# Performance work log

Measured on AMD Instinct MI355X. Metric: run time of the kernel, lower is better.

Reference implementation:

```python
import jax, jax.numpy as jnp
import numpy as np

N, E, G = 200000, 800000, 8192
IN, H, D, EXTRA = 128, 4, 64, 16


def setup_inputs() -> dict:
    key = jax.random.key(0)
    ks = jax.random.split(key, 24)
    inp = {
        'feats_node': jax.random.normal(ks[0], (N, IN), jnp.float32),
        'feats_graph': jax.random.normal(ks[1], (G, EXTRA), jnp.float32),
        'src': jax.random.randint(ks[2], (E,), 0, N, jnp.int32),
        'dst': jax.random.randint(ks[3], (E,), 0, N, jnp.int32),
        'graph_ids': jnp.sort(jax.random.randint(ks[4], (N,), 0, G, jnp.int32)),
        # GAT layer 1: fc [H*D, IN], attn [H, D], bias zeros (DGL default)
        'fc1_w': 0.5 * jax.random.normal(ks[5], (H * D, IN), jnp.float32),
        'attn_l1': 0.5 * jax.random.normal(ks[6], (H, D), jnp.float32),
        'attn_r1': 0.5 * jax.random.normal(ks[7], (H, D), jnp.float32),
        'bias1': jnp.zeros((H * D,), jnp.float32),
        # GAT layer 2
        'fc2_w': 0.5 * jax.random.normal(ks[8], (H * D, H * D), jnp.float32),
        'attn_l2': 0.5 * jax.random.normal(ks[9], (H, D), jnp.float32),
        'attn_r2': 0.5 * jax.random.normal(ks[10], (H, D), jnp.float32),
        'bias2': jnp.zeros((H * D,), jnp.float32),
        # GAT layer 3: 1 head
        'fc3_w': 0.5 * jax.random.normal(ks[11], (D, H * D), jnp.float32),
        'attn_l3': 0.5 * jax.random.normal(ks[12], (1, D), jnp.float32),
        'attn_r3': 0.5 * jax.random.normal(ks[13], (1, D), jnp.float32),
        'bias3': jnp.zeros((D,), jnp.float32),
        # readout score
        'score_w': 0.5 * jax.random.normal(ks[14], (1, D), jnp.float32),
        'score_b': jnp.zeros((1,), jnp.float32),
        # MLP: [D+EXTRA -> 2D -> D -> 1]
        'mlp_w1': 0.5 * jax.random.normal(ks[15], (2 * D, D + EXTRA), jnp.float32),
        'mlp_b1': jnp.zeros((2 * D,), jnp.float32),
        'mlp_w2': 0.5 * jax.random.normal(ks[16], (D, 2 * D), jnp.float32),
        'mlp_b2': jnp.zeros((D,), jnp.float32),
        'mlp_w3': 0.5 * jax.random.normal(ks[17], (1, D), jnp.float32),
        'mlp_b3': jnp.zeros((1,), jnp.float32),
    }
    return inp


def gat_conv(x, src, dst, fc_w, attn_l, attn_r, bias, n_heads, out_dim):
    # DGL GATConv: proj -> edge leaky_relu attention -> per-dst softmax -> aggregate
    n = x.shape[0]
    feat = (x @ fc_w.T).reshape(n, n_heads, out_dim)          # [N,H,D]
    el = jnp.einsum('nhd,hd->nh', feat, attn_l)               # [N,H]
    er = jnp.einsum('nhd,hd->nh', feat, attn_r)
    e = jax.nn.leaky_relu(el[src] + er[dst], 0.2)             # [E,H]
    m = jax.ops.segment_max(e, dst, num_segments=n)           # per-dst max
    m = jax.lax.stop_gradient(jnp.where(jnp.isfinite(m), m, 0.0))
    a = jnp.exp(e - m[dst])                                   # [E,H]
    denom = jax.ops.segment_sum(a, dst, num_segments=n)       # [N,H]
    alpha = a / jnp.where(denom[dst] == 0, 1.0, denom[dst])
    out = jax.ops.segment_sum(alpha[:, :, None] * feat[src], dst, num_segments=n)
    return out + bias.reshape(1, n_heads, out_dim)            # [N,H,D]


def reference(feats_node, feats_graph, src, dst, graph_ids,
              fc1_w, attn_l1, attn_r1, bias1,
              fc2_w, attn_l2, attn_r2, bias2,
              fc3_w, attn_l3, attn_r3, bias3,
              score_w, score_b,
              mlp_w1, mlp_b1, mlp_w2, mlp_b2, mlp_w3, mlp_b3):
    n = feats_node.shape[0]
    g = feats_graph.shape[0]
    x = jax.nn.selu(gat_conv(feats_node, src, dst, fc1_w, attn_l1, attn_r1, bias1, H, D)).reshape(n, H * D)
    x = jax.nn.selu(gat_conv(x, src, dst, fc2_w, attn_l2, attn_r2, bias2, H, D)).reshape(n, H * D)
    x = jax.nn.selu(gat_conv(x, src, dst, fc3_w, attn_l3, attn_r3, bias3, 1, D)).reshape(n, D)
    # weighted-average readout: sum(w*x)/sum(w) per graph
    w = jax.nn.sigmoid(x @ score_w.T + score_b)               # [N,1]
    num = jax.ops.segment_sum(w * x, graph_ids, num_segments=g)
    den = jax.ops.segment_sum(w, graph_ids, num_segments=g)
    emb = num / jnp.where(den == 0, 1.0, den)                 # [G,D]
    z = jnp.concatenate([emb, feats_graph], axis=1)           # [G,D+EXTRA]
    h = jax.nn.selu(z @ mlp_w1.T + mlp_b1)
    h = jax.nn.selu(h @ mlp_w2.T + mlp_b2)
    return h @ mlp_w3.T + mlp_b3                              # [G,1]
```

## Files before the change

### kernel.cpp

```cpp
#include <hip/hip_runtime.h>
#include <math.h>

#define N_NODES 200000
#define N_EDGES 800000
#define N_GRAPHS 8192
#define B1 16
#define B2 8

typedef unsigned short ushort_t;

__device__ __forceinline__ float selu_f(float x){
  const float alpha = 1.6732632423543772f;
  const float lam   = 1.0507009873554805f;
  return x > 0.f ? lam * x : lam * alpha * (expf(x) - 1.f);
}

__global__ void zero_i32(int* p, int n){
  int i = blockIdx.x * 256 + threadIdx.x;
  if (i < n) p[i] = 0;
}

__global__ void deg_kernel(const int* __restrict__ dst, int* __restrict__ deg, int E){
  int e = blockIdx.x * 256 + threadIdx.x;
  if (e < E) atomicAdd(&deg[dst[e]], 1);
}

__global__ void scan1(const int* __restrict__ deg, int* __restrict__ rp, int* __restrict__ bs, int n){
  __shared__ int sh[256];
  int t = threadIdx.x;
  int base = blockIdx.x * 1024;
  int v[4]; int s = 0;
  #pragma unroll
  for (int i = 0; i < 4; i++){
    int idx = base + t * 4 + i;
    v[i] = (idx < n) ? deg[idx] : 0;
    s += v[i];
  }
  sh[t] = s; __syncthreads();
  for (int off = 1; off < 256; off <<= 1){
    int x = (t >= off) ? sh[t - off] : 0;
    __syncthreads();
    sh[t] += x;
    __syncthreads();
  }
  int run = (t == 0) ? 0 : sh[t - 1];
  #pragma unroll
  for (int i = 0; i < 4; i++){
    int idx = base + t * 4 + i;
    if (idx < n) rp[idx] = run;
    run += v[i];
  }
  if (t == 255) bs[blockIdx.x] = sh[255];
}

__global__ void scan2(int* bs, int nb){
  __shared__ int sh[256];
  int t = threadIdx.x;
  sh[t] = (t < nb) ? bs[t] : 0; __syncthreads();
  for (int off = 1; off < 256; off <<= 1){
    int x = (t >= off) ? sh[t - off] : 0;
    __syncthreads();
    sh[t] += x;
    __syncthreads();
  }
  int excl = (t == 0) ? 0 : sh[t - 1];
  if (t < nb) bs[t] = excl;
}

__global__ void scan3(int* rp, const int* __restrict__ bs, int n, int total){
  int i = blockIdx.x * 256 + threadIdx.x;
  if (i < n) rp[i] += bs[i >> 10];
  if (i == 0) rp[n] = total;
}

__global__ void fill_csr(const int* __restrict__ src, const int* __restrict__ dst,
                         const int* __restrict__ rp, int* __restrict__ fil,
                         int* __restrict__ csr, int E){
  int e = blockIdx.x * 256 + threadIdx.x;
  if (e < E){
    int d = dst[e];
    int p = atomicAdd(&fil[d], 1);
    csr[rp[d] + p] = src[e];
  }
}

__global__ void wt_kernel(const float* __restrict__ W1, const float* __restrict__ W2,
                          const float* __restrict__ W3,
                          float* __restrict__ W1t, float* __restrict__ W2t,
                          float* __restrict__ W3t){
  int i = blockIdx.x * 256 + threadIdx.x;
  if (i < 32768){
    int k = i >> 8, m = i & 255;
    W1t[i] = W1[(size_t)m * 128 + k];
  } else if (i < 32768 + 65536){
    int j = i - 32768;
    int k = j >> 8, m = j & 255;
    W2t[j] = W2[(size_t)m * 256 + k];
  } else if (i < 32768 + 65536 + 16384){
    int j = i - 32768 - 65536;
    int k = j >> 6, c = j & 63;
    W3t[j] = W3[(size_t)c * 256 + k];
  }
}

__global__ void compute_v(const float* __restrict__ W1, const float* __restrict__ al1, const float* __restrict__ ar1,
                          const float* __restrict__ W2, const float* __restrict__ al2, const float* __restrict__ ar2,
                          const float* __restrict__ W3, const float* __restrict__ al3, const float* __restrict__ ar3,
                          float* __restrict__ V1L, float* __restrict__ V1R,
                          float* __restrict__ V2L, float* __restrict__ V2R,
                          float* __restrict__ V3L, float* __restrict__ V3R){
  int i = blockIdx.x * 256 + threadIdx.x;
  if (i < 512){
    int h = i >> 7, k = i & 127;
    float sl = 0.f, sr = 0.f;
    for (int dd = 0; dd < 64; dd++){
      float w = W1[(size_t)(h * 64 + dd) * 128 + k];
      sl += al1[h * 64 + dd] * w;
      sr += ar1[h * 64 + dd] * w;
    }
    V1L[i] = sl; V1R[i] = sr;
  } else if (i < 1536){
    int j = i - 512;
    int h = j >> 8, k = j & 255;
    float sl = 0.f, sr = 0.f;
    for (int dd = 0; dd < 64; dd++){
      float w = W2[(size_t)(h * 64 + dd) * 256 + k];
      sl += al2[h * 64 + dd] * w;
      sr += ar2[h * 64 + dd] * w;
    }
    V2L[j] = sl; V2R[j] = sr;
  } else if (i < 1792){
    int k = i - 1536;
    float sl = 0.f, sr = 0.f;
    for (int dd = 0; dd < 64; dd++){
      float w = W3[(size_t)dd * 256 + k];
      sl += al3[dd] * w;
      sr += ar3[dd] * w;
    }
    V3L[k] = sl; V3R[k] = sr;
  }
}

__global__ __launch_bounds__(256) void el_er1(const float* __restrict__ x0,
                                              const float* __restrict__ V1L, const float* __restrict__ V1R,
                                              float* __restrict__ el1, float* __restrict__ er1, int n){
  __shared__ float vl[512], vr[512];
  int t = threadIdx.x;
  for (int i = t; i < 512; i += 256){ vl[i] = V1L[i]; vr[i] = V1R[i]; }
  __syncthreads();
  int node = blockIdx.x * 4 + (t >> 6);
  int l = t & 63;
  if (node >= n) return;
  float xa = x0[(size_t)node * 128 + l];
  float xb = x0[(size_t)node * 128 + 64 + l];
  #pragma unroll
  for (int h = 0; h < 4; h++){
    float pl = xa * vl[h * 128 + l] + xb * vl[h * 128 + 64 + l];
    float pr = xa * vr[h * 128 + l] + xb * vr[h * 128 + 64 + l];
    #pragma unroll
    for (int off = 32; off; off >>= 1){ pl += __shfl_xor(pl, off); pr += __shfl_xor(pr, off); }
    if (l == 0){ el1[(size_t)node * 4 + h] = pl; er1[(size_t)node * 4 + h] = pr; }
  }
}

__global__ __launch_bounds__(256) void alpha_h4(const float* __restrict__ el, const float* __restrict__ er,
                                                const int* __restrict__ rp, const int* __restrict__ csr,
                                                float* __restrict__ a, int n){
  int node = blockIdx.x * 256 + threadIdx.x;
  if (node >= n) return;
  int s0 = rp[node], s1 = rp[node + 1];
  if (s0 >= s1) return;
  float4 erv = *reinterpret_cast<const float4*>(er + (size_t)node * 4);
  float m0 = -1e30f, m1 = -1e30f, m2 = -1e30f, m3 = -1e30f;
  for (int i = s0; i < s1; i++){
    float4 e = *reinterpret_cast<const float4*>(el + (size_t)csr[i] * 4);
    float e0 = e.x + erv.x; e0 = e0 > 0.f ? e0 : 0.2f * e0; m0 = fmaxf(m0, e0);
    float e1 = e.y + erv.y; e1 = e1 > 0.f ? e1 : 0.2f * e1; m1 = fmaxf(m1, e1);
    float e2 = e.z + erv.z; e2 = e2 > 0.f ? e2 : 0.2f * e2; m2 = fmaxf(m2, e2);
    float e3 = e.w + erv.w; e3 = e3 > 0.f ? e3 : 0.2f * e3; m3 = fmaxf(m3, e3);
  }
  float d0 = 0.f, d1 = 0.f, d2 = 0.f, d3 = 0.f;
  for (int i = s0; i < s1; i++){
    float4 e = *reinterpret_cast<const float4*>(el + (size_t)csr[i] * 4);
    float e0 = e.x + erv.x; e0 = e0 > 0.f ? e0 : 0.2f * e0; d0 += expf(e0 - m0);
    float e1 = e.y + erv.y; e1 = e1 > 0.f ? e1 : 0.2f * e1; d1 += expf(e1 - m1);
    float e2 = e.z + erv.z; e2 = e2 > 0.f ? e2 : 0.2f * e2; d2 += expf(e2 - m2);
    float e3 = e.w + erv.w; e3 = e3 > 0.f ? e3 : 0.2f * e3; d3 += expf(e3 - m3);
  }
  d0 = 1.f / d0; d1 = 1.f / d1; d2 = 1.f / d2; d3 = 1.f / d3;
  for (int i = s0; i < s1; i++){
    float4 e = *reinterpret_cast<const float4*>(el + (size_t)csr[i] * 4);
    float4 o;
    float e0 = e.x + erv.x; e0 = e0 > 0.f ? e0 : 0.2f * e0; o.x = expf(e0 - m0) * d0;
    float e1 = e.y + erv.y; e1 = e1 > 0.f ? e1 : 0.2f * e1; o.y = expf(e1 - m1) * d1;
    float e2 = e.z + erv.z; e2 = e2 > 0.f ? e2 : 0.2f * e2; o.z = expf(e2 - m2) * d2;
    float e3 = e.w + erv.w; e3 = e3 > 0.f ? e3 : 0.2f * e3; o.w = expf(e3 - m3) * d3;
    *reinterpret_cast<float4*>(a + (size_t)i * 4) = o;
  }
}

__global__ __launch_bounds__(256) void alpha_h1(const float* __restrict__ el, const float* __restrict__ er,
                                                const int* __restrict__ rp, const int* __restrict__ csr,
                                                float* __restrict__ a, int n){
  int node = blockIdx.x * 256 + threadIdx.x;
  if (node >= n) return;
  int s0 = rp[node], s1 = rp[node + 1];
  if (s0 >= s1) return;
  float erv = er[node];
  float m = -1e30f;
  for (int i = s0; i < s1; i++){
    float e = el[csr[i]] + erv; e = e > 0.f ? e : 0.2f * e; m = fmaxf(m, e);
  }
  float den = 0.f;
  for (int i = s0; i < s1; i++){
    float e = el[csr[i]] + erv; e = e > 0.f ? e : 0.2f * e; den += expf(e - m);
  }
  float inv = 1.f / den;
  for (int i = s0; i < s1; i++){
    float e = el[csr[i]] + erv; e = e > 0.f ? e : 0.2f * e; a[i] = expf(e - m) * inv;
  }
}

__global__ __launch_bounds__(512, 2) void l1_fused(
    const float* __restrict__ x0, const float* __restrict__ W1t, const float* __restrict__ bias1,
    const float* __restrict__ a1,
    const float* __restrict__ V2L, const float* __restrict__ V2R,
    const int* __restrict__ rp, const int* __restrict__ csr,
    ushort_t* __restrict__ x1hi, unsigned char* __restrict__ x1lo,
    float* __restrict__ el2, float* __restrict__ er2){
  __shared__ float aggT[4][128][20];
  __shared__ float x1s[16][260];
  int t = threadIdx.x;
  int nb0 = blockIdx.x * B1;

  {
    int g = t >> 5;
    int c4 = t & 31;
    int i0 = rp[nb0 + g], i1 = rp[nb0 + g + 1];
    float accr[4][4] = {{0.f}};
    int s = (i0 < i1) ? csr[i0] : 0;
    for (int i = i0; i < i1; i++){
      int snext = (i + 1 < i1) ? csr[i + 1] : 0;
      float4 av = *reinterpret_cast<const float4*>(a1 + (size_t)i * 4);
      float4 xv = *reinterpret_cast<const float4*>(x0 + (size_t)s * 128 + c4 * 4);
      accr[0][0] += av.x * xv.x; accr[0][1] += av.x * xv.y; accr[0][2] += av.x * xv.z; accr[0][3] += av.x * xv.w;
      accr[1][0] += av.y * xv.x; accr[1][1] += av.y * xv.y; accr[1][2] += av.y * xv.z; accr[1][3] += av.y * xv.w;
      accr[2][0] += av.z * xv.x; accr[2][1] += av.z * xv.y; accr[2][2] += av.z * xv.z; accr[2][3] += av.z * xv.w;
      accr[3][0] += av.w * xv.x; accr[3][1] += av.w * xv.y; accr[3][2] += av.w * xv.z; accr[3][3] += av.w * xv.w;
      s = snext;
    }
    #pragma unroll
    for (int h = 0; h < 4; h++)
      #pragma unroll
      for (int j = 0; j < 4; j++)
        aggT[h][c4 * 4 + j][g] = accr[h][j];
  }
  __syncthreads();

  {
    int mt = t >> 3, dp = t & 7;
    int m0 = mt * 4, h = mt >> 4;
    float acc0[4] = {0.f, 0.f, 0.f, 0.f};
    float acc1[4] = {0.f, 0.f, 0.f, 0.f};
    #pragma unroll 4
    for (int k = 0; k < 128; k++){
      float4 w = *reinterpret_cast<const float4*>(W1t + (size_t)k * 256 + m0);
      float a0 = aggT[h][k][dp];
      float a1v = aggT[h][k][dp + 8];
      acc0[0] += a0 * w.x; acc0[1] += a0 * w.y; acc0[2] += a0 * w.z; acc0[3] += a0 * w.w;
      acc1[0] += a1v * w.x; acc1[1] += a1v * w.y; acc1[2] += a1v * w.z; acc1[3] += a1v * w.w;
    }
    float4 b = *reinterpret_cast<const float4*>(bias1 + m0);
    #pragma unroll
    for (int r = 0; r < 2; r++){
      int d = dp + r * 8;
      float* ac = r ? acc1 : acc0;
      float4 v;
      v.x = selu_f(ac[0] + b.x);
      v.y = selu_f(ac[1] + b.y);
      v.z = selu_f(ac[2] + b.z);
      v.w = selu_f(ac[3] + b.w);
      *reinterpret_cast<float4*>(&x1s[d][m0]) = v;
      unsigned int ux = __float_as_uint(v.x), uy = __float_as_uint(v.y);
      unsigned int uz = __float_as_uint(v.z), uw = __float_as_uint(v.w);
      ushort4 h4; uchar4 l4;
      h4.x = (ushort_t)(ux >> 16); h4.y = (ushort_t)(uy >> 16);
      h4.z = (ushort_t)(uz >> 16); h4.w = (ushort_t)(uw >> 16);
      l4.x = (unsigned char)(ux >> 8); l4.y = (unsigned char)(uy >> 8);
      l4.z = (unsigned char)(uz >> 8); l4.w = (unsigned char)(uw >> 8);
      size_t base = (size_t)(nb0 + d) * 256 + m0;
      *reinterpret_cast<ushort4*>(x1hi + base) = h4;
      *reinterpret_cast<uchar4*>(x1lo + base) = l4;
    }
  }
  __syncthreads();

  if (t < 128){
    int d = t & 15, hq = (t >> 4) & 3, lr = t >> 6;
    const float* V = lr ? V2R : V2L;
    const float4* Vq = reinterpret_cast<const float4*>(V + hq * 256);
    const float4* Xq = reinterpret_cast<const float4*>(&x1s[d][0]);
    float p = 0.f;
    #pragma unroll 4
    for (int q = 0; q < 64; q++){
      float4 v = Vq[q]; float4 x = Xq[q];
      p += v.x * x.x; p += v.y * x.y; p += v.z * x.z; p += v.w * x.w;
    }
    if (lr) er2[(size_t)(nb0 + d) * 4 + hq] = p;
    else    el2[(size_t)(nb0 + d) * 4 + hq] = p;
  }
}

__global__ __launch_bounds__(512, 2) void l2_fused(
    const ushort_t* __restrict__ x1hi, const unsigned char* __restrict__ x1lo,
    const float* __restrict__ W2t, const float* __restrict__ bias2,
    const float* __restrict__ a2, const float* __restrict__ W3t,
    const float* __restrict__ V3L, const float* __restrict__ V3R,
    const int* __restrict__ rp, const int* __restrict__ csr,
    float* __restrict__ feat3, float* __restrict__ el3, float* __restrict__ er3){
  __shared__ float aggT[4][256][12];
  __shared__ float Wst[4160];
  __shared__ float x2s[8][260];
  int t = threadIdx.x;
  int nb0 = blockIdx.x * B2;

  {
    int d = t >> 6;
    int c4 = t & 63;
    int i0 = rp[nb0 + d], i1 = rp[nb0 + d + 1];
    float accr[4][4] = {{0.f}};
    int s = (i0 < i1) ? csr[i0] : 0;
    for (int i = i0; i < i1; i++){
      int snext = (i + 1 < i1) ? csr[i + 1] : 0;
      float4 av = *reinterpret_cast<const float4*>(a2 + (size_t)i * 4);
      ushort4 hv = *reinterpret_cast<const ushort4*>(x1hi + (size_t)s * 256 + c4 * 4);
      uchar4  lv = *reinterpret_cast<const uchar4*>(x1lo + (size_t)s * 256 + c4 * 4);
      float x0v = __uint_as_float(((unsigned int)hv.x << 16) | ((unsigned int)lv.x << 8));
      float x1v = __uint_as_float(((unsigned int)hv.y << 16) | ((unsigned int)lv.y << 8));
      float x2v = __uint_as_float(((unsigned int)hv.z << 16) | ((unsigned int)lv.z << 8));
      float x3v = __uint_as_float(((unsigned int)hv.w << 16) | ((unsigned int)lv.w << 8));
      accr[0][0] += av.x * x0v; accr[0][1] += av.x * x1v; accr[0][2] += av.x * x2v; accr[0][3] += av.x * x3v;
      accr[1][0] += av.y * x0v; accr[1][1] += av.y * x1v; accr[1][2] += av.y * x2v; accr[1][3] += av.y * x3v;
      accr[2][0] += av.z * x0v; accr[2][1] += av.z * x1v; accr[2][2] += av.z * x2v; accr[2][3] += av.z * x3v;
      accr[3][0] += av.w * x0v; accr[3][1] += av.w * x1v; accr[3][2] += av.w * x2v; accr[3][3] += av.w * x3v;
      s = snext;
    }
    #pragma unroll
    for (int h = 0; h < 4; h++)
      #pragma unroll
      for (int j = 0; j < 4; j++)
        aggT[h][c4 * 4 + j][d] = accr[h][j];
  }
  __syncthreads();

  {
    int mt = t >> 3, d2 = t & 7;
    int m0 = mt * 4, h = mt >> 4;
    float acc[4] = {0.f, 0.f, 0.f, 0.f};
    int skr = t >> 5, sm = (t * 8) & 255;
    for (int kc = 0; kc < 16; kc++){
      {
        const float* wsrc = W2t + (size_t)(kc * 16 + skr) * 256 + sm;
        float4 wa = *reinterpret_cast<const float4*>(wsrc);
        float4 wb = *reinterpret_cast<const float4*>(wsrc + 4);
        *reinterpret_cast<float4*>(&Wst[skr * 260 + sm]) = wa;
        *reinterpret_cast<float4*>(&Wst[skr * 260 + sm + 4]) = wb;
      }
      __syncthreads();
      #pragma unroll 4
      for (int kr = 0; kr < 16; kr++){
        int k = kc * 16 + kr;
        float4 w = *reinterpret_cast<const float4*>(&Wst[kr * 260 + m0]);
        float a = aggT[h][k][d2];
        acc[0] += a * w.x; acc[1] += a * w.y; acc[2] += a * w.z; acc[3] += a * w.w;
      }
      __syncthreads();
    }
    float4 b = *reinterpret_cast<const float4*>(bias2 + m0);
    float4 v;
    v.x = selu_f(acc[0] + b.x);
    v.y = selu_f(acc[1] + b.y);
    v.z = selu_f(acc[2] + b.z);
    v.w = selu_f(acc[3] + b.w);
    *reinterpret_cast<float4*>(&x2s[d2][m0]) = v;
  }
  __syncthreads();

  {
    int d3 = t >> 6, c = t & 63;
    float acc = 0.f;
    int skr = t >> 3, sc = (t * 8) & 63;
    for (int kc = 0; kc < 4; kc++){
      __syncthreads();
      {
        const float* wsrc = W3t + (size_t)(kc * 64 + skr) * 64 + sc;
        float4 wa = *reinterpret_cast<const float4*>(wsrc);
        float4 wb = *reinterpret_cast<const float4*>(wsrc + 4);
        *reinterpret_cast<float4*>(&Wst[skr * 64 + sc]) = wa;
        *reinterpret_cast<float4*>(&Wst[skr * 64 + sc + 4]) = wb;
      }
      __syncthreads();
      #pragma unroll 8
      for (int kr = 0; kr < 64; kr++){
        acc += Wst[kr * 64 + c] * x2s[d3][kc * 64 + kr];
      }
    }
    feat3[(size_t)(nb0 + d3) * 64 + c] = acc;
  }

  if (t < 16){
    int d = t & 7, lr = t >> 3;
    const float* V = lr ? V3R : V3L;
    float p = 0.f;
    for (int k = 0; k < 256; k++) p += V[k] * x2s[d][k];
    if (lr) er3[nb0 + d] = p;
    else    el3[nb0 + d] = p;
  }
}

__global__ __launch_bounds__(256) void gat_agg3(const float* __restrict__ feat, const float* __restrict__ a3,
                                                const int* __restrict__ rp, const int* __restrict__ csr,
                                                const float* __restrict__ bias,
                                                float* __restrict__ out, int n){
  int node = blockIdx.x * 4 + (threadIdx.x >> 6);
  int t = threadIdx.x & 63;
  if (node >= n) return;
  int s0 = rp[node], s1 = rp[node + 1];
  float acc = 0.f;
  int s = (s0 < s1) ? csr[s0] : 0;
  for (int i = s0; i < s1; i++){
    int snext = (i + 1 < s1) ? csr[i + 1] : 0;
    acc += a3[i] * feat[(size_t)s * 64 + t];
    s = snext;
  }
  out[(size_t)node * 64 + t] = selu_f(acc + bias[t]);
}

__global__ void readout_kernel(const float* __restrict__ x3, const float* __restrict__ score_w,
                               const float* __restrict__ score_b, const int* __restrict__ gids,
                               float* __restrict__ num, float* __restrict__ den, int n){
  int node = blockIdx.x * 4 + (threadIdx.x >> 6);
  int lane = threadIdx.x & 63;
  if (node >= n) return;
  float xv = x3[(size_t)node * 64 + lane];
  float p = xv * score_w[lane];
  #pragma unroll
  for (int off = 32; off; off >>= 1) p += __shfl_xor(p, off);
  float w = 1.f / (1.f + expf(-(p + score_b[0])));
  int g = gids[node];
  atomicAdd(&num[(size_t)g * 64 + lane], w * xv);
  if (lane == 0) atomicAdd(&den[g], w);
}

__global__ __launch_bounds__(128) void mlp_kernel(
    const float* __restrict__ num, const float* __restrict__ den,
    const float* __restrict__ fg,
    const float* __restrict__ w1, const float* __restrict__ b1,
    const float* __restrict__ w2, const float* __restrict__ b2,
    const float* __restrict__ w3, const float* __restrict__ b3,
    float* __restrict__ out, int G){
  __shared__ float z[80];
  __shared__ float h1[128];
  __shared__ float h2[64];
  int t = threadIdx.x;
  for (int g = blockIdx.x; g < G; g += gridDim.x){
    if (t < 64){
      float d = den[g];
      d = (d == 0.f) ? 1.f : d;
      z[t] = num[(size_t)g * 64 + t] / d;
    } else if (t < 80){
      z[t] = fg[(size_t)g * 16 + (t - 64)];
    }
    __syncthreads();
    {
      float a = b1[t];
      for (int k = 0; k < 80; k++) a += z[k] * w1[t * 80 + k];
      h1[t] = selu_f(a);
    }
    __syncthreads();
    if (t < 64){
      float a = b2[t];
      for (int k = 0; k < 128; k++) a += h1[k] * w2[t * 128 + k];
      h2[t] = selu_f(a);
    }
    __syncthreads();
    if (t < 64){
      float p = h2[t] * w3[t];
      #pragma unroll
      for (int off = 32; off; off >>= 1) p += __shfl_down(p, off);
      if (t == 0) out[g] = p + b3[0];
    }
    __syncthreads();
  }
}

extern "C" void kernel_launch(void* const* d_in, const int* in_sizes, int n_in,
                              void* d_out, int out_size, void* d_ws, size_t ws_size,
                              hipStream_t stream) {
  const float* feats_node  = (const float*)d_in[0];
  const float* feats_graph = (const float*)d_in[1];
  const int*   src         = (const int*)d_in[2];
  const int*   dst         = (const int*)d_in[3];
  const int*   gids        = (const int*)d_in[4];
  const float* fc1_w   = (const float*)d_in[5];
  const float* attn_l1 = (const float*)d_in[6];
  const float* attn_r1 = (const float*)d_in[7];
  const float* bias1   = (const float*)d_in[8];
  const float* fc2_w   = (const float*)d_in[9];
  const float* attn_l2 = (const float*)d_in[10];
  const float* attn_r2 = (const float*)d_in[11];
  const float* bias2   = (const float*)d_in[12];
  const float* fc3_w   = (const float*)d_in[13];
  const float* attn_l3 = (const float*)d_in[14];
  const float* attn_r3 = (const float*)d_in[15];
  const float* bias3   = (const float*)d_in[16];
  const float* score_w = (const float*)d_in[17];
  const float* score_b = (const float*)d_in[18];
  const float* mlp_w1  = (const float*)d_in[19];
  const float* mlp_b1  = (const float*)d_in[20];
  const float* mlp_w2  = (const float*)d_in[21];
  const float* mlp_b2  = (const float*)d_in[22];
  const float* mlp_w3  = (const float*)d_in[23];
  const float* mlp_b3  = (const float*)d_in[24];
  float* out = (float*)d_out;

  char* ws = (char*)d_ws;
  size_t off = 0;
  auto alloc = [&](size_t bytes) -> void* {
    void* p = ws + off;
    off += (bytes + 255) / 256 * 256;
    return p;
  };
  int*   deg   = (int*)alloc((size_t)N_NODES * 4);
  int*   fil   = (int*)alloc((size_t)N_NODES * 4);
  int*   rp    = (int*)alloc((size_t)(N_NODES + 1) * 4);
  int*   bs    = (int*)alloc(256 * 4);
  int*   csr   = (int*)alloc((size_t)N_EDGES * 4);
  float* elbuf = (float*)alloc((size_t)N_NODES * 4 * 4);
  float* erbuf = (float*)alloc((size_t)N_NODES * 4 * 4);
  float* V1L   = (float*)alloc(512 * 4);
  float* V1R   = (float*)alloc(512 * 4);
  float* V2L   = (float*)alloc(1024 * 4);
  float* V2R   = (float*)alloc(1024 * 4);
  float* V3L   = (float*)alloc(256 * 4);
  float* V3R   = (float*)alloc(256 * 4);
  float* W1t   = (float*)alloc(32768 * 4);
  float* W2t   = (float*)alloc(65536 * 4);
  float* W3t   = (float*)alloc(16384 * 4);
  float* num   = (float*)alloc((size_t)N_GRAPHS * 64 * 4);
  float* den   = (float*)alloc((size_t)N_GRAPHS * 4);
  float* A     = (float*)alloc((size_t)N_EDGES * 4 * 4);
  float* feat3 = (float*)alloc((size_t)N_NODES * 64 * 4);
  ushort_t*      x1hi = (ushort_t*)alloc((size_t)N_NODES * 256 * 2);
  unsigned char* x1lo = (unsigned char*)alloc((size_t)N_NODES * 256);
  float* x3 = (float*)x1hi;

  zero_i32<<<(N_NODES + 255) / 256, 256, 0, stream>>>(deg, N_NODES);
  zero_i32<<<(N_NODES + 255) / 256, 256, 0, stream>>>(fil, N_NODES);
  zero_i32<<<(N_GRAPHS * 64 + 255) / 256, 256, 0, stream>>>((int*)num, N_GRAPHS * 64);
  zero_i32<<<(N_GRAPHS + 255) / 256, 256, 0, stream>>>((int*)den, N_GRAPHS);

  deg_kernel<<<(N_EDGES + 255) / 256, 256, 0, stream>>>(dst, deg, N_EDGES);
  scan1<<<196, 256, 0, stream>>>(deg, rp, bs, N_NODES);
  scan2<<<1, 256, 0, stream>>>(bs, 196);
  scan3<<<(N_NODES + 255) / 256, 256, 0, stream>>>(rp, bs, N_NODES, N_EDGES);
  fill_csr<<<(N_EDGES + 255) / 256, 256, 0, stream>>>(src, dst, rp, fil, csr, N_EDGES);

  compute_v<<<7, 256, 0, stream>>>(fc1_w, attn_l1, attn_r1, fc2_w, attn_l2, attn_r2,
                                   fc3_w, attn_l3, attn_r3, V1L, V1R, V2L, V2R, V3L, V3R);
  wt_kernel<<<448, 256, 0, stream>>>(fc1_w, fc2_w, fc3_w, W1t, W2t, W3t);
  el_er1<<<N_NODES / 4, 256, 0, stream>>>(feats_node, V1L, V1R, elbuf, erbuf, N_NODES);

  alpha_h4<<<(N_NODES + 255) / 256, 256, 0, stream>>>(elbuf, erbuf, rp, csr, A, N_NODES);
  l1_fused<<<N_NODES / B1, 512, 0, stream>>>(feats_node, W1t, bias1, A,
                                             V2L, V2R, rp, csr, x1hi, x1lo, elbuf, erbuf);
  alpha_h4<<<(N_NODES + 255) / 256, 256, 0, stream>>>(elbuf, erbuf, rp, csr, A, N_NODES);
  l2_fused<<<N_NODES / B2, 512, 0, stream>>>(x1hi, x1lo, W2t, bias2, A, W3t,
                                             V3L, V3R, rp, csr, feat3, elbuf, erbuf);
  alpha_h1<<<(N_NODES + 255) / 256, 256, 0, stream>>>(elbuf, erbuf, rp, csr, A, N_NODES);
  gat_agg3<<<N_NODES / 4, 256, 0, stream>>>(feat3, A, rp, csr, bias3, x3, N_NODES);

  readout_kernel<<<N_NODES / 4, 256, 0, stream>>>(x3, score_w, score_b, gids, num, den, N_NODES);
  mlp_kernel<<<256, 128, 0, stream>>>(num, den, feats_graph,
                                      mlp_w1, mlp_b1, mlp_w2, mlp_b2, mlp_w3, mlp_b3,
                                      out, N_GRAPHS);
}
```

Before: 2.597 ms.

## Restructure fused GAT layer GEMMs to read untransposed weights with node-major smem

Result: slower. 3.269 ms (+25.9%).

```diff
diff --git a/kernel.cpp b/kernel.cpp
--- a/kernel.cpp
+++ b/kernel.cpp
@@ -5,7 +5,7 @@
 #define N_EDGES 800000
 #define N_GRAPHS 8192
 #define B1 16
-#define B2 8
+#define B2 16
 
 typedef unsigned short ushort_t;
 
@@ -81,25 +81,6 @@
     int d = dst[e];
     int p = atomicAdd(&fil[d], 1);
     csr[rp[d] + p] = src[e];
-  }
-}
-
-__global__ void wt_kernel(const float* __restrict__ W1, const float* __restrict__ W2,
-                          const float* __restrict__ W3,
-                          float* __restrict__ W1t, float* __restrict__ W2t,
-                          float* __restrict__ W3t){
-  int i = blockIdx.x * 256 + threadIdx.x;
-  if (i < 32768){
-    int k = i >> 8, m = i & 255;
-    W1t[i] = W1[(size_t)m * 128 + k];
-  } else if (i < 32768 + 65536){
-    int j = i - 32768;
-    int k = j >> 8, m = j & 255;
-    W2t[j] = W2[(size_t)m * 256 + k];
-  } else if (i < 32768 + 65536 + 16384){
-    int j = i - 32768 - 65536;
-    int k = j >> 6, c = j & 63;
-    W3t[j] = W3[(size_t)c * 256 + k];
   }
 }
 
@@ -221,15 +202,15 @@
   }
 }
 
-__global__ __launch_bounds__(512, 2) void l1_fused(
-    const float* __restrict__ x0, const float* __restrict__ W1t, const float* __restrict__ bias1,
+__global__ __launch_bounds__(512, 4) void l1_fused(
+    const float* __restrict__ x0, const float* __restrict__ W1, const float* __restrict__ bias1,
     const float* __restrict__ a1,
     const float* __restrict__ V2L, const float* __restrict__ V2R,
     const int* __restrict__ rp, const int* __restrict__ csr,
     ushort_t* __restrict__ x1hi, unsigned char* __restrict__ x1lo,
     float* __restrict__ el2, float* __restrict__ er2){
-  __shared__ float aggT[4][128][20];
-  __shared__ float x1s[16][260];
+  __shared__ float aggT[4][B1][132];
+  float* x1s = &aggT[0][0][0];
   int t = threadIdx.x;
   int nb0 = blockIdx.x * B1;
 
@@ -240,47 +221,58 @@
     float accr[4][4] = {{0.f}};
     int s = (i0 < i1) ? csr[i0] : 0;
     for (int i = i0; i < i1; i++){
-      int snext = (i + 1 < i1) ? csr[i + 1] : 0;
+      int sn = (i + 1 < i1) ? csr[i + 1] : 0;
       float4 av = *reinterpret_cast<const float4*>(a1 + (size_t)i * 4);
       float4 xv = *reinterpret_cast<const float4*>(x0 + (size_t)s * 128 + c4 * 4);
       accr[0][0] += av.x * xv.x; accr[0][1] += av.x * xv.y; accr[0][2] += av.x * xv.z; accr[0][3] += av.x * xv.w;
       accr[1][0] += av.y * xv.x; accr[1][1] += av.y * xv.y; accr[1][2] += av.y * xv.z; accr[1][3] += av.y * xv.w;
       accr[2][0] += av.z * xv.x; accr[2][1] += av.z * xv.y; accr[2][2] += av.z * xv.z; accr[2][3] += av.z * xv.w;
       accr[3][0] += av.w * xv.x; accr[3][1] += av.w * xv.y; accr[3][2] += av.w * xv.z; accr[3][3] += av.w * xv.w;
-      s = snext;
+      s = sn;
     }
     #pragma unroll
-    for (int h = 0; h < 4; h++)
+    for (int h = 0; h < 4; h++){
+      float4 v = make_float4(accr[h][0], accr[h][1], accr[h][2], accr[h][3]);
+      *reinterpret_cast<float4*>(&aggT[h][g][c4 * 4]) = v;
+    }
+  }
+  __syncthreads();
+
+  {
+    int mq = t >> 2, dq = t & 3;
+    int m0 = mq * 2;
+    int h = m0 >> 6;
+    float acc[2][4] = {{0.f}};
+    const float* w0p = W1 + (size_t)m0 * 128;
+    #pragma unroll 4
+    for (int kq = 0; kq < 32; kq++){
+      int k = kq * 4;
+      float4 w0 = *reinterpret_cast<const float4*>(w0p + k);
+      float4 w1 = *reinterpret_cast<const float4*>(w0p + 128 + k);
       #pragma unroll
-      for (int j = 0; j < 4; j++)
-        aggT[h][c4 * 4 + j][g] = accr[h][j];
+      for (int r = 0; r < 4; r++){
+        float4 a = *reinterpret_cast<const float4*>(&aggT[h][dq + 4 * r][k]);
+        acc[0][r] += w0.x * a.x + w0.y * a.y + w0.z * a.z + w0.w * a.w;
+        acc[1][r] += w1.x * a.x + w1.y * a.y + w1.z * a.z + w1.w * a.w;
+      }
+    }
+    float b0 = bias1[m0], b1 = bias1[m0 + 1];
+    __syncthreads();
+    #pragma unroll
+    for (int r = 0; r < 4; r++){
+      int d = dq + 4 * r;
+      x1s[d * 260 + m0]     = selu_f(acc[0][r] + b0);
+      x1s[d * 260 + m0 + 1] = selu_f(acc[1][r] + b1);
+    }
   }
   __syncthreads();
 
   {
-    int mt = t >> 3, dp = t & 7;
-    int m0 = mt * 4, h = mt >> 4;
-    float acc0[4] = {0.f, 0.f, 0.f, 0.f};
-    float acc1[4] = {0.f, 0.f, 0.f, 0.f};
-    #pragma unroll 4
-    for (int k = 0; k < 128; k++){
-      float4 w = *reinterpret_cast<const float4*>(W1t + (size_t)k * 256 + m0);
-      float a0 = aggT[h][k][dp];
-      float a1v = aggT[h][k][dp + 8];
-      acc0[0] += a0 * w.x; acc0[1] += a0 * w.y; acc0[2] += a0 * w.z; acc0[3] += a0 * w.w;
-      acc1[0] += a1v * w.x; acc1[1] += a1v * w.y; acc1[2] += a1v * w.z; acc1[3] += a1v * w.w;
-    }
-    float4 b = *reinterpret_cast<const float4*>(bias1 + m0);
+    int row = t >> 5, cq = t & 31;
     #pragma unroll
-    for (int r = 0; r < 2; r++){
-      int d = dp + r * 8;
-      float* ac = r ? acc1 : acc0;
-      float4 v;
-      v.x = selu_f(ac[0] + b.x);
-      v.y = selu_f(ac[1] + b.y);
-      v.z = selu_f(ac[2] + b.z);
-      v.w = selu_f(ac[3] + b.w);
-      *reinterpret_cast<float4*>(&x1s[d][m0]) = v;
+    for (int it = 0; it < 2; it++){
+      int c4 = cq + it * 32;
+      float4 v = *reinterpret_cast<float4*>(&x1s[row * 260 + c4 * 4]);
       unsigned int ux = __float_as_uint(v.x), uy = __float_as_uint(v.y);
       unsigned int uz = __float_as_uint(v.z), uw = __float_as_uint(v.w);
       ushort4 h4; uchar4 l4;
@@ -288,18 +280,17 @@
       h4.z = (ushort_t)(uz >> 16); h4.w = (ushort_t)(uw >> 16);
       l4.x = (unsigned char)(ux >> 8); l4.y = (unsigned char)(uy >> 8);
       l4.z = (unsigned char)(uz >> 8); l4.w = (unsigned char)(uw >> 8);
-      size_t base = (size_t)(nb0 + d) * 256 + m0;
+      size_t base = (size_t)(nb0 + row) * 256 + c4 * 4;
       *reinterpret_cast<ushort4*>(x1hi + base) = h4;
       *reinterpret_cast<uchar4*>(x1lo + base) = l4;
     }
   }
-  __syncthreads();
 
   if (t < 128){
     int d = t & 15, hq = (t >> 4) & 3, lr = t >> 6;
     const float* V = lr ? V2R : V2L;
     const float4* Vq = reinterpret_cast<const float4*>(V + hq * 256);
-    const float4* Xq = reinterpret_cast<const float4*>(&x1s[d][0]);
+    const float4* Xq = reinterpret_cast<const float4*>(&x1s[d * 260]);
     float p = 0.f;
     #pragma unroll 4
     for (int q = 0; q < 64; q++){
@@ -311,110 +302,115 @@
   }
 }
 
-__global__ __launch_bounds__(512, 2) void l2_fused(
+__global__ __launch_bounds__(512, 4) void l2_fused(
     const ushort_t* __restrict__ x1hi, const unsigned char* __restrict__ x1lo,
-    const float* __restrict__ W2t, const float* __restrict__ bias2,
-    const float* __restrict__ a2, const float* __restrict__ W3t,
+    const float* __restrict__ W2, const float* __restrict__ bias2,
+    const float* __restrict__ a2, const float* __restrict__ W3,
     const float* __restrict__ V3L, const float* __restrict__ V3R,
     const int* __restrict__ rp, const int* __restrict__ csr,
     float* __restrict__ feat3, float* __restrict__ el3, float* __restrict__ er3){
-  __shared__ float aggT[4][256][12];
-  __shared__ float Wst[4160];
-  __shared__ float x2s[8][260];
+  __shared__ float aggT[4][B2][260];
+  float* x2s = &aggT[0][0][0];
   int t = threadIdx.x;
   int nb0 = blockIdx.x * B2;
 
   {
-    int d = t >> 6;
-    int c4 = t & 63;
-    int i0 = rp[nb0 + d], i1 = rp[nb0 + d + 1];
-    float accr[4][4] = {{0.f}};
+    int g = t >> 5;
+    int l4 = t & 31;
+    int i0 = rp[nb0 + g], i1 = rp[nb0 + g + 1];
+    float accr[4][8] = {{0.f}};
     int s = (i0 < i1) ? csr[i0] : 0;
     for (int i = i0; i < i1; i++){
-      int snext = (i + 1 < i1) ? csr[i + 1] : 0;
+      int sn = (i + 1 < i1) ? csr[i + 1] : 0;
       float4 av = *reinterpret_cast<const float4*>(a2 + (size_t)i * 4);
-      ushort4 hv = *reinterpret_cast<const ushort4*>(x1hi + (size_t)s * 256 + c4 * 4);
-      uchar4  lv = *reinterpret_cast<const uchar4*>(x1lo + (size_t)s * 256 + c4 * 4);
-      float x0v = __uint_as_float(((unsigned int)hv.x << 16) | ((unsigned int)lv.x << 8));
-      float x1v = __uint_as_float(((unsigned int)hv.y << 16) | ((unsigned int)lv.y << 8));
-      float x2v = __uint_as_float(((unsigned int)hv.z << 16) | ((unsigned int)lv.z << 8));
-      float x3v = __uint_as_float(((unsigned int)hv.w << 16) | ((unsigned int)lv.w << 8));
-      accr[0][0] += av.x * x0v; accr[0][1] += av.x * x1v; accr[0][2] += av.x * x2v; accr[0][3] += av.x * x3v;
-      accr[1][0] += av.y * x0v; accr[1][1] += av.y * x1v; accr[1][2] += av.y * x2v; accr[1][3] += av.y * x3v;
-      accr[2][0] += av.z * x0v; accr[2][1] += av.z * x1v; accr[2][2] += av.z * x2v; accr[2][3] += av.z * x3v;
-      accr[3][0] += av.w * x0v; accr[3][1] += av.w * x1v; accr[3][2] += av.w * x2v; accr[3][3] += av.w * x3v;
-      s = snext;
+      #pragma unroll
+      for (int seg = 0; seg < 2; seg++){
+        size_t off = (size_t)s * 256 + seg * 128 + l4 * 4;
+        ushort4 hv = *reinterpret_cast<const ushort4*>(x1hi + off);
+        uchar4  lv = *reinterpret_cast<const uchar4*>(x1lo + off);
+        float x0v = __uint_as_float(((unsigned int)hv.x << 16) | ((unsigned int)lv.x << 8));
+        float x1v = __uint_as_float(((unsigned int)hv.y << 16) | ((unsigned int)lv.y << 8));
+        float x2v = __uint_as_float(((unsigned int)hv.z << 16) | ((unsigned int)lv.z << 8));
+        float x3v = __uint_as_float(((unsigned int)hv.w << 16) | ((unsigned int)lv.w << 8));
+        accr[0][seg * 4 + 0] += av.x * x0v; accr[0][seg * 4 + 1] += av.x * x1v;
+        accr[0][seg * 4 + 2] += av.x * x2v; accr[0][seg * 4 + 3] += av.x * x3v;
+        accr[1][seg * 4 + 0] += av.y * x0v; accr[1][seg * 4 + 1] += av.y * x1v;
+        accr[1][seg * 4 + 2] += av.y * x2v; accr[1][seg * 4 + 3] += av.y * x3v;
+        accr[2][seg * 4 + 0] += av.z * x0v; accr[2][seg * 4 + 1] += av.z * x1v;
+        accr[2][seg * 4 + 2] += av.z * x2v; accr[2][seg * 4 + 3] += av.z * x3v;
+        accr[3][seg * 4 + 0] += av.w * x0v; accr[3][seg * 4 + 1] += av.w * x1v;
+        accr[3][seg * 4 + 2] += av.w * x2v; accr[3][seg * 4 + 3] += av.w * x3v;
+      }
+      s = sn;
     }
     #pragma unroll
     for (int h = 0; h < 4; h++)
       #pragma unroll
-      for (int j = 0; j < 4; j++)
-        aggT[h][c4 * 4 + j][d] = accr[h][j];
+      for (int seg = 0; seg < 2; seg++){
+        float4 v = make_float4(accr[h][seg * 4 + 0], accr[h][seg * 4 + 1],
+                               accr[h][seg * 4 + 2], accr[h][seg * 4 + 3]);
+        *reinterpret_cast<float4*>(&aggT[h][g][seg * 128 + l4 * 4]) = v;
+      }
   }
   __syncthreads();
 
   {
-    int mt = t >> 3, d2 = t & 7;
-    int m0 = mt * 4, h = mt >> 4;
-    float acc[4] = {0.f, 0.f, 0.f, 0.f};
-    int skr = t >> 5, sm = (t * 8) & 255;
-    for (int kc = 0; kc < 16; kc++){
-      {
-        const float* wsrc = W2t + (size_t)(kc * 16 + skr) * 256 + sm;
-        float4 wa = *reinterpret_cast<const float4*>(wsrc);
-        float4 wb = *reinterpret_cast<const float4*>(wsrc + 4);
-        *reinterpret_cast<float4*>(&Wst[skr * 260 + sm]) = wa;
-        *reinterpret_cast<float4*>(&Wst[skr * 260 + sm + 4]) = wb;
+    int mq = t >> 2, dq = t & 3;
+    int m0 = mq * 2;
+    int h = m0 >> 6;
+    float acc[2][4] = {{0.f}};
+    const float* w0p = W2 + (size_t)m0 * 256;
+    #pragma unroll 2
+    for (int kq = 0; kq < 64; kq++){
+      int k = kq * 4;
+      float4 w0 = *reinterpret_cast<const float4*>(w0p + k);
+      float4 w1 = *reinterpret_cast<const float4*>(w0p + 256 + k);
+      #pragma unroll
+      for (int r = 0; r < 4; r++){
+        float4 a = *reinterpret_cast<const float4*>(&aggT[h][dq + 4 * r][k]);
+        acc[0][r] += w0.x * a.x + w0.y * a.y + w0.z * a.z + w0.w * a.w;
+        acc[1][r] += w1.x * a.x + w1.y * a.y + w1.z * a.z + w1.w * a.w;
       }
-      __syncthreads();
-      #pragma unroll 4
-      for (int kr = 0; kr < 16; kr++){
-        int k = kc * 16 + kr;
-        float4 w = *reinterpret_cast<const float4*>(&Wst[kr * 260 + m0]);
-        float a = aggT[h][k][d2];
-        acc[0] += a * w.x; acc[1] += a * w.y; acc[2] += a * w.z; acc[3] += a * w.w;
-      }
-      __syncthreads();
-    }
-    float4 b = *reinterpret_cast<const float4*>(bias2 + m0);
-    float4 v;
-    v.x = selu_f(acc[0] + b.x);
-    v.y = selu_f(acc[1] + b.y);
-    v.z = selu_f(acc[2] + b.z);
-    v.w = selu_f(acc[3] + b.w);
-    *reinterpret_cast<float4*>(&x2s[d2][m0]) = v;
+    }
+    float b0 = bias2[m0], b1 = bias2[m0 + 1];
+    __syncthreads();
+    #pragma unroll
+    for (int r = 0; r < 4; r++){
+      int d = dq + 4 * r;
+      x2s[d * 260 + m0]     = selu_f(acc[0][r] + b0);
+      x2s[d * 260 + m0 + 1] = selu_f(acc[1][r] + b1);
+    }
   }
   __syncthreads();
 
-  {
-    int d3 = t >> 6, c = t & 63;
-    float acc = 0.f;
-    int skr = t >> 3, sc = (t * 8) & 63;
-    for (int kc = 0; kc < 4; kc++){
-      __syncthreads();
-      {
-        const float* wsrc = W3t + (size_t)(kc * 64 + skr) * 64 + sc;
-        float4 wa = *reinterpret_cast<const float4*>(wsrc);
-        float4 wb = *reinterpret_cast<const float4*>(wsrc + 4);
-        *reinterpret_cast<float4*>(&Wst[skr * 64 + sc]) = wa;
-        *reinterpret_cast<float4*>(&Wst[skr * 64 + sc + 4]) = wb;
-      }
-      __syncthreads();
-      #pragma unroll 8
-      for (int kr = 0; kr < 64; kr++){
-        acc += Wst[kr * 64 + c] * x2s[d3][kc * 64 + kr];
-      }
-    }
-    feat3[(size_t)(nb0 + d3) * 64 + c] = acc;
-  }
-
-  if (t < 16){
-    int d = t & 7, lr = t >> 3;
+  if (t < 128){
+    int q = t & 3, d = (t >> 2) & 15, lr = t >> 6;
     const float* V = lr ? V3R : V3L;
     float p = 0.f;
-    for (int k = 0; k < 256; k++) p += V[k] * x2s[d][k];
-    if (lr) er3[nb0 + d] = p;
-    else    el3[nb0 + d] = p;
+    for (int kk = 0; kk < 64; kk++){
+      int k = q + kk * 4;
+      p += V[k] * x2s[d * 260 + k];
+    }
+    p += __shfl_xor(p, 1); p += __shfl_xor(p, 2);
+    if (q == 0){ if (lr) er3[nb0 + d] = p; else el3[nb0 + d] = p; }
+  }
+
+  {
+    int d = t >> 5, c2 = t & 31;
+    int c = c2 * 2;
+    float acc0 = 0.f, acc1 = 0.f;
+    const float* w0p = W3 + (size_t)c * 256;
+    #pragma unroll 4
+    for (int kq = 0; kq < 64; kq++){
+      int k = kq * 4;
+      float4 xr = *reinterpret_cast<const float4*>(&x2s[d * 260 + k]);
+      float4 w0 = *reinterpret_cast<const float4*>(w0p + k);
+      float4 w1 = *reinterpret_cast<const float4*>(w0p + 256 + k);
+      acc0 += w0.x * xr.x + w0.y * xr.y + w0.z * xr.z + w0.w * xr.w;
+      acc1 += w1.x * xr.x + w1.y * xr.y + w1.z * xr.z + w1.w * xr.w;
+    }
+    float2 o; o.x = acc0; o.y = acc1;
+    *reinterpret_cast<float2*>(feat3 + (size_t)(nb0 + d) * 64 + c) = o;
   }
 }
 
@@ -429,9 +425,9 @@
   float acc = 0.f;
   int s = (s0 < s1) ? csr[s0] : 0;
   for (int i = s0; i < s1; i++){
-    int snext = (i + 1 < s1) ? csr[i + 1] : 0;
+    int sn = (i + 1 < s1) ? csr[i + 1] : 0;
     acc += a3[i] * feat[(size_t)s * 64 + t];
-    s = snext;
+    s = sn;
   }
   out[(size_t)node * 64 + t] = selu_f(acc + bias[t]);
 }
@@ -544,9 +540,6 @@
   float* V2R   = (float*)alloc(1024 * 4);
   float* V3L   = (float*)alloc(256 * 4);
   float* V3R   = (float*)alloc(256 * 4);
-  float* W1t   = (float*)alloc(32768 * 4);
-  float* W2t   = (float*)alloc(65536 * 4);
-  float* W3t   = (float*)alloc(16384 * 4);
   float* num   = (float*)alloc((size_t)N_GRAPHS * 64 * 4);
   float* den   = (float*)alloc((size_t)N_GRAPHS * 4);
   float* A     = (float*)alloc((size_t)N_EDGES * 4 * 4);
@@ -568,14 +561,13 @@
 
   compute_v<<<7, 256, 0, stream>>>(fc1_w, attn_l1, attn_r1, fc2_w, attn_l2, attn_r2,
                                    fc3_w, attn_l3, attn_r3, V1L, V1R, V2L, V2R, V3L, V3R);
-  wt_kernel<<<448, 256, 0, stream>>>(fc1_w, fc2_w, fc3_w, W1t, W2t, W3t);
   el_er1<<<N_NODES / 4, 256, 0, stream>>>(feats_node, V1L, V1R, elbuf, erbuf, N_NODES);
 
   alpha_h4<<<(N_NODES + 255) / 256, 256, 0, stream>>>(elbuf, erbuf, rp, csr, A, N_NODES);
-  l1_fused<<<N_NODES / B1, 512, 0, stream>>>(feats_node, W1t, bias1, A,
+  l1_fused<<<N_NODES / B1, 512, 0, stream>>>(feats_node, fc1_w, bias1, A,
                                              V2L, V2R, rp, csr, x1hi, x1lo, elbuf, erbuf);
   alpha_h4<<<(N_NODES + 255) / 256, 256, 0, stream>>>(elbuf, erbuf, rp, csr, A, N_NODES);
-  l2_fused<<<N_NODES / B2, 512, 0, stream>>>(x1hi, x1lo, W2t, bias2, A, W3t,
+  l2_fused<<<N_NODES / B2, 512, 0, stream>>>(x1hi, x1lo, fc2_w, bias2, A, fc3_w,
                                              V3L, V3R, rp, csr, feat3, elbuf, erbuf);
   alpha_h1<<<(N_NODES + 255) / 256, 256, 0, stream>>>(elbuf, erbuf, rp, csr, A, N_NODES);
   gat_agg3<<<N_NODES / 4, 256, 0, stream>>>(feat3, A, rp, csr, bias3, x3, N_NODES);
```
